# Kernel tuning notes

Hardware: AMD Instinct MI355X
Metric: run time of the kernel (lower is better)

The kernel has to match this reference:

```python
import jax, jax.numpy as jnp
import numpy as np

EPS = 1e-5

def layer_norm(x, gamma, beta):
    mu = jnp.mean(x, axis=-1, keepdims=True)
    var = jnp.mean((x - mu) ** 2, axis=-1, keepdims=True)
    return (x - mu) * jax.lax.rsqrt(var + EPS) * gamma + beta

def setup_inputs() -> dict:
    key = jax.random.key(0)
    ks = jax.random.split(key, 12)
    N, E, D, B = 100000, 1200000, 64, 1
    x_h = jax.random.normal(ks[0], (N, D), dtype=jnp.float32)
    edge_index = jax.random.randint(ks[1], (2, E), 0, N, dtype=jnp.int64)
    edge_attr_h = jax.random.normal(ks[2], (E, D), dtype=jnp.float32)
    u = jax.random.normal(ks[3], (B, 1), dtype=jnp.float32)
    batch = jnp.zeros((N,), dtype=jnp.int64)
    s = 0.05
    W1 = jax.random.normal(ks[4], (2 * D, D), dtype=jnp.float32) * s
    b1 = jnp.zeros((D,), dtype=jnp.float32)
    g1 = jnp.ones((D,), dtype=jnp.float32); be1 = jnp.zeros((D,), dtype=jnp.float32)
    W2 = jax.random.normal(ks[5], (2 * D + 1, D), dtype=jnp.float32) * s
    b2 = jnp.zeros((D,), dtype=jnp.float32)
    g2 = jnp.ones((D,), dtype=jnp.float32); be2 = jnp.zeros((D,), dtype=jnp.float32)
    W3 = jax.random.normal(ks[6], (D, D), dtype=jnp.float32) * s
    b3 = jnp.zeros((D,), dtype=jnp.float32)
    g3 = jnp.ones((D,), dtype=jnp.float32); be3 = jnp.zeros((D,), dtype=jnp.float32)
    return {"x_h": x_h, "edge_index": edge_index, "edge_attr_h": edge_attr_h, "u": u, "batch": batch,
            "W1": W1, "b1": b1, "g1": g1, "be1": be1,
            "W2": W2, "b2": b2, "g2": g2, "be2": be2,
            "W3": W3, "b3": b3, "g3": g3, "be3": be3}

def reference(x_h, edge_index, edge_attr_h, u, batch,
              W1, b1, g1, be1, W2, b2, g2, be2, W3, b3, g3, be3):
    N = x_h.shape[0]
    row, col = edge_index[0], edge_index[1]
    # gather source node features, concat with edge features -> mlp1
    m = jnp.concatenate([x_h[row], edge_attr_h], axis=1)            # [E, 2D]
    m = layer_norm(jax.nn.relu(m @ W1 + b1), g1, be1)               # [E, D]
    # scatter_mean over destination nodes
    summed = jax.ops.segment_sum(m, col, num_segments=N)            # [N, D]
    cnt = jax.ops.segment_sum(jnp.ones((m.shape[0],), m.dtype), col, num_segments=N)
    agg = summed / jnp.maximum(cnt, 1.0)[:, None]                   # [N, D]
    h = jnp.concatenate([x_h, agg, u[batch]], axis=1)               # [N, 2D+1]
    h = layer_norm(jax.nn.relu(h @ W2 + b2), g2, be2)
    h = layer_norm(h @ W3 + b3, g3, be3)
    return h + x_h
```

## Files before the change

### kernel.cpp

```cpp
#include <hip/hip_runtime.h>

#define EPS 1e-5f

typedef __attribute__((ext_vector_type(8))) short short8v;
typedef __attribute__((ext_vector_type(4))) float f32x4;

__device__ __forceinline__ unsigned short f2bf(float f) {
    unsigned u = __builtin_bit_cast(unsigned, f);
    u += 0x7fffu + ((u >> 16) & 1u);
    return (unsigned short)(u >> 16);
}
__device__ __forceinline__ float bf2f(unsigned short h) {
    return __builtin_bit_cast(float, (unsigned)h << 16);
}

__global__ __launch_bounds__(256) void prep_kernel(const float* __restrict__ x,
                                                   unsigned short* __restrict__ xbf,
                                                   float* __restrict__ zbase,
                                                   long zn4, long n8) {
    long i = (long)blockIdx.x * blockDim.x + threadIdx.x;
    long stride = (long)gridDim.x * blockDim.x;
    float4* z4 = (float4*)zbase;
    for (long k = i; k < zn4; k += stride) z4[k] = make_float4(0.f, 0.f, 0.f, 0.f);
    const float4* x4 = (const float4*)x;
    for (long k = i; k < n8; k += stride) {
        float4 a = x4[2 * k], b = x4[2 * k + 1];
        short8v v;
        v[0] = (short)f2bf(a.x); v[1] = (short)f2bf(a.y);
        v[2] = (short)f2bf(a.z); v[3] = (short)f2bf(a.w);
        v[4] = (short)f2bf(b.x); v[5] = (short)f2bf(b.y);
        v[6] = (short)f2bf(b.z); v[7] = (short)f2bf(b.w);
        ((short8v*)xbf)[k] = v;
    }
}

__global__ __launch_bounds__(256) void hist_kernel(const int* __restrict__ col,
                                                   int* __restrict__ cnt, long E) {
    for (long e = (long)blockIdx.x * 256 + threadIdx.x; e < E; e += (long)gridDim.x * 256)
        atomicAdd(&cnt[col[e]], 1);
}

__global__ __launch_bounds__(256) void scan1_kernel(const int* __restrict__ cnt,
                                                    int* __restrict__ offs,
                                                    int* __restrict__ partials, int N) {
    __shared__ int sdata[256];
    int t = threadIdx.x;
    int i0 = blockIdx.x * 1024 + t * 4;
    int c[4]; int tot = 0;
    #pragma unroll
    for (int j = 0; j < 4; ++j) { c[j] = (i0 + j < N) ? cnt[i0 + j] : 0; tot += c[j]; }
    sdata[t] = tot; __syncthreads();
    for (int d = 1; d < 256; d <<= 1) {
        int v = (t >= d) ? sdata[t - d] : 0;
        __syncthreads();
        sdata[t] += v;
        __syncthreads();
    }
    int run = sdata[t] - tot;
    #pragma unroll
    for (int j = 0; j < 4; ++j) { if (i0 + j < N) offs[i0 + j] = run; run += c[j]; }
    if (t == 255) partials[blockIdx.x] = sdata[255];
}

__global__ __launch_bounds__(256) void scan2_kernel(int* __restrict__ partials, int nb) {
    __shared__ int sdata[256];
    int t = threadIdx.x;
    int v = (t < nb) ? partials[t] : 0;
    sdata[t] = v; __syncthreads();
    for (int d = 1; d < 256; d <<= 1) {
        int w = (t >= d) ? sdata[t - d] : 0;
        __syncthreads();
        sdata[t] += w;
        __syncthreads();
    }
    if (t < nb) partials[t] = sdata[t] - v;
}

__global__ __launch_bounds__(256) void scan3_kernel(int* __restrict__ offs,
                                                    int* __restrict__ head,
                                                    const int* __restrict__ partials, int N) {
    int base = partials[blockIdx.x];
    int i0 = blockIdx.x * 1024 + threadIdx.x * 4;
    #pragma unroll
    for (int j = 0; j < 4; ++j) {
        int i = i0 + j;
        if (i < N) { int v = offs[i] + base; offs[i] = v; head[i] = v; }
    }
}

__global__ __launch_bounds__(256) void permscat_kernel(const int* __restrict__ row,
                                                       const int* __restrict__ col,
                                                       int* __restrict__ head,
                                                       int2* __restrict__ einfo,
                                                       int* __restrict__ dsts, long E) {
    for (long e = (long)blockIdx.x * 256 + threadIdx.x; e < E; e += (long)gridDim.x * 256) {
        int cdst = col[e];
        int pos = atomicAdd(&head[cdst], 1);
        einfo[pos] = make_int2((int)e, row[e]);
        dsts[pos] = cdst;
    }
}

__global__ __launch_bounds__(256) void edge_kernel(
    const unsigned short* __restrict__ xbf, const float* __restrict__ eattr,
    const int2* __restrict__ einfo, const int* __restrict__ dsts,
    const float* __restrict__ W1, const float* __restrict__ b1,
    const float* __restrict__ g1, const float* __restrict__ be1,
    unsigned short* __restrict__ summed,
    int E, int N)
{
    __shared__ unsigned short T[4][64][72];
    __shared__ int dseg[4][64];

    const int lane = threadIdx.x & 63;
    const int wid  = threadIdx.x >> 6;
    const int c = lane & 15;
    const int q = lane >> 4;

    short8v w1f[4][4];
    #pragma unroll
    for (int ks = 0; ks < 4; ++ks) {
        #pragma unroll
        for (int nt = 0; nt < 4; ++nt) {
            int k0 = ks * 32 + q * 8;
            int n  = nt * 16 + c;
            short8v f;
            #pragma unroll
            for (int j = 0; j < 8; ++j) f[j] = (short)f2bf(W1[(k0 + j) * 64 + n]);
            w1f[ks][nt] = f;
        }
    }
    float b1v[4], g1v[4], bev[4];
    #pragma unroll
    for (int nt = 0; nt < 4; ++nt) {
        b1v[nt] = b1[nt * 16 + c];
        g1v[nt] = g1[nt * 16 + c];
        bev[nt] = be1[nt * 16 + c];
    }

    for (long e0 = (long)blockIdx.x * 256 + wid * 64; e0 < E; e0 += (long)gridDim.x * 256) {
        long el = e0 + lane;
        bool valid = el < E;
        int2 ps = valid ? einfo[el] : make_int2(0, 0);
        int pe = ps.x;
        int sv = ps.y;
        int dv = valid ? dsts[el] : -1;

        int prev = __shfl_up(dv, 1);
        int seg  = (lane > 0 && dv != prev) ? 1 : 0;
        int rank = seg;
        #pragma unroll
        for (int d = 1; d < 64; d <<= 1) {
            int v = __shfl_up(rank, d);
            if (lane >= d) rank += v;
        }
        int nseg = __shfl(rank, 63) + 1;
        if (lane == 0 || seg) dseg[wid][rank] = dv;

        #pragma unroll
        for (int mt = 0; mt < 4; ++mt) {
            int src  = __shfl(sv, mt * 16 + c);
            int pidx = __shfl(pe, mt * 16 + c);
            const unsigned short* xp = xbf + (long)src * 64;
            const float* ep = eattr + (long)pidx * 64;

            f32x4 acc[4];
            #pragma unroll
            for (int nt = 0; nt < 4; ++nt) acc[nt] = (f32x4){0.f, 0.f, 0.f, 0.f};

            #pragma unroll
            for (int ks = 0; ks < 2; ++ks) {
                short8v a = *(const short8v*)(xp + ks * 32 + q * 8);
                #pragma unroll
                for (int nt = 0; nt < 4; ++nt)
                    acc[nt] = __builtin_amdgcn_mfma_f32_16x16x32_bf16(
                        a, w1f[ks][nt], acc[nt], 0, 0, 0);
            }
            #pragma unroll
            for (int ks = 2; ks < 4; ++ks) {
                int k0 = (ks - 2) * 32 + q * 8;
                float4 lo = *(const float4*)(ep + k0);
                float4 hi = *(const float4*)(ep + k0 + 4);
                short8v a;
                a[0] = (short)f2bf(lo.x); a[1] = (short)f2bf(lo.y);
                a[2] = (short)f2bf(lo.z); a[3] = (short)f2bf(lo.w);
                a[4] = (short)f2bf(hi.x); a[5] = (short)f2bf(hi.y);
                a[6] = (short)f2bf(hi.z); a[7] = (short)f2bf(hi.w);
                #pragma unroll
                for (int nt = 0; nt < 4; ++nt)
                    acc[nt] = __builtin_amdgcn_mfma_f32_16x16x32_bf16(
                        a, w1f[ks][nt], acc[nt], 0, 0, 0);
            }

            float s1[4] = {0, 0, 0, 0}, s2[4] = {0, 0, 0, 0};
            #pragma unroll
            for (int nt = 0; nt < 4; ++nt)
                #pragma unroll
                for (int r = 0; r < 4; ++r) {
                    float f = fmaxf(acc[nt][r] + b1v[nt], 0.f);
                    acc[nt][r] = f;
                    s1[r] += f; s2[r] += f * f;
                }
            #pragma unroll
            for (int m = 1; m <= 8; m <<= 1)
                #pragma unroll
                for (int r = 0; r < 4; ++r) {
                    s1[r] += __shfl_xor(s1[r], m);
                    s2[r] += __shfl_xor(s2[r], m);
                }
            #pragma unroll
            for (int r = 0; r < 4; ++r) {
                float mu = s1[r] * (1.f / 64.f);
                float var = s2[r] * (1.f / 64.f) - mu * mu;
                float rs = rsqrtf(var + EPS);
                #pragma unroll
                for (int nt = 0; nt < 4; ++nt) {
                    float h = (acc[nt][r] - mu) * rs * g1v[nt] + bev[nt];
                    T[wid][nt * 16 + c][mt * 16 + q * 4 + r] = f2bf(h);
                }
            }
        }

        short8v bfr[2][4];
        #pragma unroll
        for (int ks = 0; ks < 2; ++ks)
            #pragma unroll
            for (int nt = 0; nt < 4; ++nt)
                bfr[ks][nt] = *(const short8v*)&T[wid][nt * 16 + c][ks * 32 + q * 8];

        const short ONE = (short)0x3F80;
        #pragma unroll
        for (int mt = 0; mt < 4; ++mt) {
            if (mt * 16 < nseg) {
                f32x4 acc2[4];
                #pragma unroll
                for (int nt = 0; nt < 4; ++nt) acc2[nt] = (f32x4){0.f, 0.f, 0.f, 0.f};

                #pragma unroll
                for (int ks = 0; ks < 2; ++ks) {
                    short8v af;
                    #pragma unroll
                    for (int j = 0; j < 8; ++j) {
                        int rk = __shfl(rank, ks * 32 + q * 8 + j);
                        af[j] = (rk == mt * 16 + c) ? ONE : (short)0;
                    }
                    #pragma unroll
                    for (int nt = 0; nt < 4; ++nt)
                        acc2[nt] = __builtin_amdgcn_mfma_f32_16x16x32_bf16(
                            af, bfr[ks][nt], acc2[nt], 0, 0, 0);
                }

                #pragma unroll
                for (int r = 0; r < 4; ++r) {
                    int s = mt * 16 + q * 4 + r;
                    #pragma unroll
                    for (int nt = 0; nt < 4; ++nt) {
                        float val = acc2[nt][r];
                        float nb = __shfl_xor(val, 1);
                        if (s < nseg && !(c & 1)) {
                            int dst = dseg[wid][s];
                            if (dst >= 0) {
                                unsigned pk = (unsigned)f2bf(val) | ((unsigned)f2bf(nb) << 16);
                                unsigned long long a64 = (unsigned long long)
                                    (summed + (long)dst * 64 + nt * 16 + c);
                                asm volatile("global_atomic_pk_add_bf16 %0, %1, off"
                                             :: "v"(a64), "v"(pk));
                            }
                        }
                    }
                }
            }
        }
    }
}

__global__ __launch_bounds__(256) void node_kernel(
    const float* __restrict__ x_h, const float* __restrict__ u,
    const float* __restrict__ W2, const float* __restrict__ b2,
    const float* __restrict__ g2, const float* __restrict__ be2,
    const float* __restrict__ W3, const float* __restrict__ b3,
    const float* __restrict__ g3, const float* __restrict__ be3,
    const unsigned short* __restrict__ summed, const int* __restrict__ cnt,
    float* __restrict__ out, int N)
{
    __shared__ unsigned short sh[4][64][72];

    const int lane = threadIdx.x & 63;
    const int wid  = threadIdx.x >> 6;
    const int c = lane & 15;
    const int q = lane >> 4;
    const float u0 = u[0];

    short8v w2f[4][4], w3f[2][4];
    #pragma unroll
    for (int ks = 0; ks < 4; ++ks)
        #pragma unroll
        for (int nt = 0; nt < 4; ++nt) {
            int k0 = ks * 32 + q * 8;
            int n  = nt * 16 + c;
            short8v f;
            #pragma unroll
            for (int j = 0; j < 8; ++j) f[j] = (short)f2bf(W2[(k0 + j) * 64 + n]);
            w2f[ks][nt] = f;
        }
    #pragma unroll
    for (int ks = 0; ks < 2; ++ks)
        #pragma unroll
        for (int nt = 0; nt < 4; ++nt) {
            int k0 = ks * 32 + q * 8;
            int n  = nt * 16 + c;
            short8v f;
            #pragma unroll
            for (int j = 0; j < 8; ++j) f[j] = (short)f2bf(W3[(k0 + j) * 64 + n]);
            w3f[ks][nt] = f;
        }

    float b2p[4], g2v[4], be2v[4], b3v[4], g3v[4], be3v[4];
    #pragma unroll
    for (int nt = 0; nt < 4; ++nt) {
        int n = nt * 16 + c;
        b2p[nt] = b2[n] + u0 * W2[128 * 64 + n];
        g2v[nt] = g2[n]; be2v[nt] = be2[n];
        b3v[nt] = b3[n]; g3v[nt] = g3[n]; be3v[nt] = be3[n];
    }

    const long n0 = ((long)blockIdx.x * 4 + wid) * 64;
    if (n0 >= N) return;

    #pragma unroll
    for (int mt = 0; mt < 4; ++mt) {
        long nr = n0 + mt * 16 + c;
        long nc = (nr < N) ? nr : (N - 1);
        const float* xp = x_h + nc * 64;
        const unsigned short* sp = summed + nc * 64;
        float inv = 1.f / fmaxf((float)cnt[nc], 1.f);

        f32x4 acc[4];
        #pragma unroll
        for (int nt = 0; nt < 4; ++nt) acc[nt] = (f32x4){0.f, 0.f, 0.f, 0.f};

        #pragma unroll
        for (int ks = 0; ks < 4; ++ks) {
            int k0 = ks * 32 + q * 8;
            short8v a;
            if (ks < 2) {
                float4 lo = *(const float4*)(xp + k0);
                float4 hi = *(const float4*)(xp + k0 + 4);
                a[0] = (short)f2bf(lo.x); a[1] = (short)f2bf(lo.y);
                a[2] = (short)f2bf(lo.z); a[3] = (short)f2bf(lo.w);
                a[4] = (short)f2bf(hi.x); a[5] = (short)f2bf(hi.y);
                a[6] = (short)f2bf(hi.z); a[7] = (short)f2bf(hi.w);
            } else {
                short8v raw = *(const short8v*)(sp + (k0 - 64));
                #pragma unroll
                for (int j = 0; j < 8; ++j)
                    a[j] = (short)f2bf(bf2f((unsigned short)raw[j]) * inv);
            }
            #pragma unroll
            for (int nt = 0; nt < 4; ++nt)
                acc[nt] = __builtin_amdgcn_mfma_f32_16x16x32_bf16(a, w2f[ks][nt], acc[nt], 0, 0, 0);
        }

        float s1[4] = {0, 0, 0, 0}, s2[4] = {0, 0, 0, 0};
        #pragma unroll
        for (int nt = 0; nt < 4; ++nt)
            #pragma unroll
            for (int r = 0; r < 4; ++r) {
                float f = fmaxf(acc[nt][r] + b2p[nt], 0.f);
                acc[nt][r] = f;
                s1[r] += f; s2[r] += f * f;
            }
        #pragma unroll
        for (int m = 1; m <= 8; m <<= 1)
            #pragma unroll
            for (int r = 0; r < 4; ++r) {
                s1[r] += __shfl_xor(s1[r], m);
                s2[r] += __shfl_xor(s2[r], m);
            }
        #pragma unroll
        for (int r = 0; r < 4; ++r) {
            float mu = s1[r] * (1.f / 64.f);
            float var = s2[r] * (1.f / 64.f) - mu * mu;
            float rs = rsqrtf(var + EPS);
            #pragma unroll
            for (int nt = 0; nt < 4; ++nt) {
                float h2 = (acc[nt][r] - mu) * rs * g2v[nt] + be2v[nt];
                sh[wid][mt * 16 + q * 4 + r][nt * 16 + c] = f2bf(h2);
            }
        }
    }

    #pragma unroll
    for (int mt = 0; mt < 4; ++mt) {
        f32x4 acc[4];
        #pragma unroll
        for (int nt = 0; nt < 4; ++nt) acc[nt] = (f32x4){0.f, 0.f, 0.f, 0.f};

        #pragma unroll
        for (int ks = 0; ks < 2; ++ks) {
            short8v a = *(const short8v*)&sh[wid][mt * 16 + c][ks * 32 + q * 8];
            #pragma unroll
            for (int nt = 0; nt < 4; ++nt)
                acc[nt] = __builtin_amdgcn_mfma_f32_16x16x32_bf16(a, w3f[ks][nt], acc[nt], 0, 0, 0);
        }

        float s1[4] = {0, 0, 0, 0}, s2[4] = {0, 0, 0, 0};
        #pragma unroll
        for (int nt = 0; nt < 4; ++nt)
            #pragma unroll
            for (int r = 0; r < 4; ++r) {
                float f = acc[nt][r] + b3v[nt];
                acc[nt][r] = f;
                s1[r] += f; s2[r] += f * f;
            }
        #pragma unroll
        for (int m = 1; m <= 8; m <<= 1)
            #pragma unroll
            for (int r = 0; r < 4; ++r) {
                s1[r] += __shfl_xor(s1[r], m);
                s2[r] += __shfl_xor(s2[r], m);
            }
        #pragma unroll
        for (int r = 0; r < 4; ++r) {
            float mu = s1[r] * (1.f / 64.f);
            float var = s2[r] * (1.f / 64.f) - mu * mu;
            float rs = rsqrtf(var + EPS);
            long node = n0 + mt * 16 + q * 4 + r;
            if (node < N) {
                #pragma unroll
                for (int nt = 0; nt < 4; ++nt) {
                    long off = node * 64 + nt * 16 + c;
                    float h3 = (acc[nt][r] - mu) * rs * g3v[nt] + be3v[nt];
                    out[off] = h3 + x_h[off];
                }
            }
        }
    }
}

extern "C" void kernel_launch(void* const* d_in, const int* in_sizes, int n_in,
                              void* d_out, int out_size, void* d_ws, size_t ws_size,
                              hipStream_t stream)
{
    const float* x_h   = (const float*)d_in[0];
    const int*   eidx  = (const int*)  d_in[1];
    const float* eattr = (const float*)d_in[2];
    const float* u     = (const float*)d_in[3];
    const float* W1  = (const float*)d_in[5];
    const float* b1  = (const float*)d_in[6];
    const float* g1  = (const float*)d_in[7];
    const float* be1 = (const float*)d_in[8];
    const float* W2  = (const float*)d_in[9];
    const float* b2  = (const float*)d_in[10];
    const float* g2  = (const float*)d_in[11];
    const float* be2 = (const float*)d_in[12];
    const float* W3  = (const float*)d_in[13];
    const float* b3  = (const float*)d_in[14];
    const float* g3  = (const float*)d_in[15];
    const float* be3 = (const float*)d_in[16];

    const int N = in_sizes[0] / 64;
    const int E = in_sizes[1] / 2;
    const int* row = eidx;
    const int* col = eidx + E;

    char* w = (char*)d_ws;
    unsigned short* xbf    = (unsigned short*)w;   w += (size_t)N * 128;
    unsigned short* summed = (unsigned short*)w;   w += (size_t)N * 128;
    int* cnt      = (int*)w;                       w += (size_t)N * 4;
    int* offs     = (int*)w;                       w += (size_t)N * 4;
    int* head     = (int*)w;                       w += (size_t)N * 4;
    int* dsts     = (int*)w;                       w += (size_t)E * 4;
    int2* einfo   = (int2*)w;                      w += (size_t)E * 8;
    int* partials = (int*)w;

    prep_kernel<<<1024, 256, 0, stream>>>(x_h, xbf, (float*)summed, ((long)N * 33) / 4, (long)N * 8);

    hist_kernel<<<2048, 256, 0, stream>>>(col, cnt, E);
    int sblocks = (N + 1023) / 1024;
    scan1_kernel<<<sblocks, 256, 0, stream>>>(cnt, offs, partials, N);
    scan2_kernel<<<1, 256, 0, stream>>>(partials, sblocks);
    scan3_kernel<<<sblocks, 256, 0, stream>>>(offs, head, partials, N);
    permscat_kernel<<<2048, 256, 0, stream>>>(row, col, head, einfo, dsts, E);

    int tiles = (E + 63) / 64;
    int eblocks = (tiles + 7) / 8;
    edge_kernel<<<eblocks, 256, 0, stream>>>(xbf, eattr, einfo, dsts,
                                             W1, b1, g1, be1, summed, E, N);

    int nblocks = (N + 255) / 256;
    node_kernel<<<nblocks, 256, 0, stream>>>(x_h, u, W2, b2, g2, be2, W3, b3, g3, be3,
                                             summed, cnt, (float*)d_out, N);
}
```

Baseline: 358.8 us.

## Split edge MLP from aggregation; compute MLP in original edge order, aggregate sorted

After: 330.8 us. 7.8% less time.

```diff
diff --git a/kernel.cpp b/kernel.cpp
--- a/kernel.cpp
+++ b/kernel.cpp
@@ -88,11 +88,23 @@
     }
 }
 
-__global__ __launch_bounds__(256) void permscat_kernel(const int* __restrict__ row,
-                                                       const int* __restrict__ col,
-                                                       int* __restrict__ head,
-                                                       int2* __restrict__ einfo,
-                                                       int* __restrict__ dsts, long E) {
+__global__ __launch_bounds__(256) void permscat2_kernel(const int* __restrict__ col,
+                                                        int* __restrict__ head,
+                                                        int* __restrict__ perm,
+                                                        int* __restrict__ dsts, long E) {
+    for (long e = (long)blockIdx.x * 256 + threadIdx.x; e < E; e += (long)gridDim.x * 256) {
+        int cdst = col[e];
+        int pos = atomicAdd(&head[cdst], 1);
+        perm[pos] = (int)e;
+        dsts[pos] = cdst;
+    }
+}
+
+__global__ __launch_bounds__(256) void permscat_r9_kernel(const int* __restrict__ row,
+                                                          const int* __restrict__ col,
+                                                          int* __restrict__ head,
+                                                          int2* __restrict__ einfo,
+                                                          int* __restrict__ dsts, long E) {
     for (long e = (long)blockIdx.x * 256 + threadIdx.x; e < E; e += (long)gridDim.x * 256) {
         int cdst = col[e];
         int pos = atomicAdd(&head[cdst], 1);
@@ -101,7 +113,164 @@
     }
 }
 
-__global__ __launch_bounds__(256) void edge_kernel(
+__global__ __launch_bounds__(256) void mlp_kernel(
+    const unsigned short* __restrict__ xbf, const int* __restrict__ eidx,
+    const float* __restrict__ eattr,
+    const float* __restrict__ W1, const float* __restrict__ b1,
+    const float* __restrict__ g1, const float* __restrict__ be1,
+    unsigned short* __restrict__ m, int* __restrict__ cnt, int E)
+{
+    const int lane = threadIdx.x & 63;
+    const int wid  = threadIdx.x >> 6;
+    const int c = lane & 15;
+    const int q = lane >> 4;
+
+    short8v w1f[4][4];
+    #pragma unroll
+    for (int ks = 0; ks < 4; ++ks)
+        #pragma unroll
+        for (int nt = 0; nt < 4; ++nt) {
+            int k0 = ks * 32 + q * 8;
+            int n  = nt * 16 + c;
+            short8v f;
+            #pragma unroll
+            for (int j = 0; j < 8; ++j) f[j] = (short)f2bf(W1[(k0 + j) * 64 + n]);
+            w1f[ks][nt] = f;
+        }
+    float b1v[4], g1v[4], bev[4];
+    #pragma unroll
+    for (int nt = 0; nt < 4; ++nt) {
+        b1v[nt] = b1[nt * 16 + c];
+        g1v[nt] = g1[nt * 16 + c];
+        bev[nt] = be1[nt * 16 + c];
+    }
+
+    for (long e0 = (long)blockIdx.x * 256 + wid * 64; e0 < E; e0 += (long)gridDim.x * 256) {
+        int sv_l;
+        {
+            long el = e0 + lane;
+            if (el < E) atomicAdd(&cnt[eidx[E + el]], 1);
+            sv_l = (el < E) ? eidx[el] : 0;
+        }
+
+        #pragma unroll
+        for (int mt = 0; mt < 4; ++mt) {
+            long er = e0 + mt * 16 + c;
+            long ec = (er < E) ? er : (E - 1);
+            int src = __shfl(sv_l, mt * 16 + c);
+            const unsigned short* xp = xbf + (long)src * 64;
+            const float* ep = eattr + ec * 64;
+
+            f32x4 acc[4];
+            #pragma unroll
+            for (int nt = 0; nt < 4; ++nt) acc[nt] = (f32x4){0.f, 0.f, 0.f, 0.f};
+
+            #pragma unroll
+            for (int ks = 0; ks < 2; ++ks) {
+                short8v a = *(const short8v*)(xp + ks * 32 + q * 8);
+                #pragma unroll
+                for (int nt = 0; nt < 4; ++nt)
+                    acc[nt] = __builtin_amdgcn_mfma_f32_16x16x32_bf16(
+                        a, w1f[ks][nt], acc[nt], 0, 0, 0);
+            }
+            #pragma unroll
+            for (int ks = 2; ks < 4; ++ks) {
+                int k0 = (ks - 2) * 32 + q * 8;
+                float4 lo = *(const float4*)(ep + k0);
+                float4 hi = *(const float4*)(ep + k0 + 4);
+                short8v a;
+                a[0] = (short)f2bf(lo.x); a[1] = (short)f2bf(lo.y);
+                a[2] = (short)f2bf(lo.z); a[3] = (short)f2bf(lo.w);
+                a[4] = (short)f2bf(hi.x); a[5] = (short)f2bf(hi.y);
+                a[6] = (short)f2bf(hi.z); a[7] = (short)f2bf(hi.w);
+                #pragma unroll
+                for (int nt = 0; nt < 4; ++nt)
+                    acc[nt] = __builtin_amdgcn_mfma_f32_16x16x32_bf16(
+                        a, w1f[ks][nt], acc[nt], 0, 0, 0);
+            }
+
+            float s1[4] = {0, 0, 0, 0}, s2[4] = {0, 0, 0, 0};
+            #pragma unroll
+            for (int nt = 0; nt < 4; ++nt)
+                #pragma unroll
+                for (int r = 0; r < 4; ++r) {
+                    float f = fmaxf(acc[nt][r] + b1v[nt], 0.f);
+                    acc[nt][r] = f;
+                    s1[r] += f; s2[r] += f * f;
+                }
+            #pragma unroll
+            for (int mm = 1; mm <= 8; mm <<= 1)
+                #pragma unroll
+                for (int r = 0; r < 4; ++r) {
+                    s1[r] += __shfl_xor(s1[r], mm);
+                    s2[r] += __shfl_xor(s2[r], mm);
+                }
+            #pragma unroll
+            for (int r = 0; r < 4; ++r) {
+                float mu = s1[r] * (1.f / 64.f);
+                float var = s2[r] * (1.f / 64.f) - mu * mu;
+                float rs = rsqrtf(var + EPS);
+                long ee = e0 + mt * 16 + q * 4 + r;
+                #pragma unroll
+                for (int nt = 0; nt < 4; ++nt) {
+                    float h = (acc[nt][r] - mu) * rs * g1v[nt] + bev[nt];
+                    float nb = __shfl_xor(h, 1);
+                    if (ee < E && !(c & 1)) {
+                        unsigned pk = (unsigned)f2bf(h) | ((unsigned)f2bf(nb) << 16);
+                        *(unsigned*)(m + ee * 64 + nt * 16 + c) = pk;
+                    }
+                }
+            }
+        }
+    }
+}
+
+__global__ __launch_bounds__(256, 8) void agg_kernel(
+    const unsigned short* __restrict__ m, const int* __restrict__ perm,
+    const int* __restrict__ dsts, unsigned short* __restrict__ summed, int E)
+{
+    const int lane = threadIdx.x & 63;
+    const int wid  = threadIdx.x >> 6;
+
+    for (long s0 = ((long)blockIdx.x * 4 + wid) * 64; s0 < E; s0 += (long)gridDim.x * 256) {
+        long sl = s0 + lane;
+        int pe_l = (sl < E) ? perm[sl] : 0;
+        int dv_l = (sl < E) ? dsts[sl] : -1;
+
+        float acc = 0.f;
+        #pragma unroll
+        for (int base = 0; base < 64; base += 8) {
+            int pe8[8], dv8[8]; float v[8];
+            #pragma unroll
+            for (int j = 0; j < 8; ++j) {
+                pe8[j] = __shfl(pe_l, base + j);
+                dv8[j] = __shfl(dv_l, base + j);
+            }
+            int dvn = (base < 56) ? __shfl(dv_l, base + 8) : (int)0x80000000;
+            #pragma unroll
+            for (int j = 0; j < 8; ++j)
+                v[j] = bf2f(m[(long)pe8[j] * 64 + lane]);
+            #pragma unroll
+            for (int j = 0; j < 8; ++j) {
+                if (dv8[j] >= 0) acc += v[j];
+                int nxt = (j < 7) ? dv8[j + 1] : dvn;
+                if (nxt != dv8[j]) {
+                    float nb = __shfl_xor(acc, 1);
+                    if (dv8[j] >= 0 && !(lane & 1)) {
+                        unsigned pk = (unsigned)f2bf(acc) | ((unsigned)f2bf(nb) << 16);
+                        unsigned long long a64 = (unsigned long long)
+                            (summed + (long)dv8[j] * 64 + lane);
+                        asm volatile("global_atomic_pk_add_bf16 %0, %1, off"
+                                     :: "v"(a64), "v"(pk));
+                    }
+                    acc = 0.f;
+                }
+            }
+        }
+    }
+}
+
+__global__ __launch_bounds__(256) void edge_kernel_r9(
     const unsigned short* __restrict__ xbf, const float* __restrict__ eattr,
     const int2* __restrict__ einfo, const int* __restrict__ dsts,
     const float* __restrict__ W1, const float* __restrict__ b1,
@@ -119,7 +288,7 @@
 
     short8v w1f[4][4];
     #pragma unroll
-    for (int ks = 0; ks < 4; ++ks) {
+    for (int ks = 0; ks < 4; ++ks)
         #pragma unroll
         for (int nt = 0; nt < 4; ++nt) {
             int k0 = ks * 32 + q * 8;
@@ -129,7 +298,6 @@
             for (int j = 0; j < 8; ++j) f[j] = (short)f2bf(W1[(k0 + j) * 64 + n]);
             w1f[ks][nt] = f;
         }
-    }
     float b1v[4], g1v[4], bev[4];
     #pragma unroll
     for (int nt = 0; nt < 4; ++nt) {
@@ -142,8 +310,7 @@
         long el = e0 + lane;
         bool valid = el < E;
         int2 ps = valid ? einfo[el] : make_int2(0, 0);
-        int pe = ps.x;
-        int sv = ps.y;
+        int pe = ps.x, sv = ps.y;
         int dv = valid ? dsts[el] : -1;
 
         int prev = __shfl_up(dv, 1);
@@ -202,11 +369,11 @@
                     s1[r] += f; s2[r] += f * f;
                 }
             #pragma unroll
-            for (int m = 1; m <= 8; m <<= 1)
+            for (int mmm = 1; mmm <= 8; mmm <<= 1)
                 #pragma unroll
                 for (int r = 0; r < 4; ++r) {
-                    s1[r] += __shfl_xor(s1[r], m);
-                    s2[r] += __shfl_xor(s2[r], m);
+                    s1[r] += __shfl_xor(s1[r], mmm);
+                    s2[r] += __shfl_xor(s2[r], mmm);
                 }
             #pragma unroll
             for (int r = 0; r < 4; ++r) {
@@ -235,7 +402,6 @@
                 f32x4 acc2[4];
                 #pragma unroll
                 for (int nt = 0; nt < 4; ++nt) acc2[nt] = (f32x4){0.f, 0.f, 0.f, 0.f};
-
                 #pragma unroll
                 for (int ks = 0; ks < 2; ++ks) {
                     short8v af;
@@ -249,7 +415,6 @@
                         acc2[nt] = __builtin_amdgcn_mfma_f32_16x16x32_bf16(
                             af, bfr[ks][nt], acc2[nt], 0, 0, 0);
                 }
-
                 #pragma unroll
                 for (int r = 0; r < 4; ++r) {
                     int s = mt * 16 + q * 4 + r;
@@ -371,11 +536,11 @@
                 s1[r] += f; s2[r] += f * f;
             }
         #pragma unroll
-        for (int m = 1; m <= 8; m <<= 1)
+        for (int mm = 1; mm <= 8; mm <<= 1)
             #pragma unroll
             for (int r = 0; r < 4; ++r) {
-                s1[r] += __shfl_xor(s1[r], m);
-                s2[r] += __shfl_xor(s2[r], m);
+                s1[r] += __shfl_xor(s1[r], mm);
+                s2[r] += __shfl_xor(s2[r], mm);
             }
         #pragma unroll
         for (int r = 0; r < 4; ++r) {
@@ -414,11 +579,11 @@
                 s1[r] += f; s2[r] += f * f;
             }
         #pragma unroll
-        for (int m = 1; m <= 8; m <<= 1)
+        for (int mm = 1; mm <= 8; mm <<= 1)
             #pragma unroll
             for (int r = 0; r < 4; ++r) {
-                s1[r] += __shfl_xor(s1[r], m);
-                s2[r] += __shfl_xor(s2[r], m);
+                s1[r] += __shfl_xor(s1[r], mm);
+                s2[r] += __shfl_xor(s2[r], mm);
             }
         #pragma unroll
         for (int r = 0; r < 4; ++r) {
@@ -464,31 +629,60 @@
     const int* row = eidx;
     const int* col = eidx + E;
 
-    char* w = (char*)d_ws;
-    unsigned short* xbf    = (unsigned short*)w;   w += (size_t)N * 128;
-    unsigned short* summed = (unsigned short*)w;   w += (size_t)N * 128;
-    int* cnt      = (int*)w;                       w += (size_t)N * 4;
-    int* offs     = (int*)w;                       w += (size_t)N * 4;
-    int* head     = (int*)w;                       w += (size_t)N * 4;
-    int* dsts     = (int*)w;                       w += (size_t)E * 4;
-    int2* einfo   = (int2*)w;                      w += (size_t)E * 8;
-    int* partials = (int*)w;
-
-    prep_kernel<<<1024, 256, 0, stream>>>(x_h, xbf, (float*)summed, ((long)N * 33) / 4, (long)N * 8);
-
-    hist_kernel<<<2048, 256, 0, stream>>>(col, cnt, E);
-    int sblocks = (N + 1023) / 1024;
-    scan1_kernel<<<sblocks, 256, 0, stream>>>(cnt, offs, partials, N);
-    scan2_kernel<<<1, 256, 0, stream>>>(partials, sblocks);
-    scan3_kernel<<<sblocks, 256, 0, stream>>>(offs, head, partials, N);
-    permscat_kernel<<<2048, 256, 0, stream>>>(row, col, head, einfo, dsts, E);
-
-    int tiles = (E + 63) / 64;
-    int eblocks = (tiles + 7) / 8;
-    edge_kernel<<<eblocks, 256, 0, stream>>>(xbf, eattr, einfo, dsts,
-                                             W1, b1, g1, be1, summed, E, N);
-
-    int nblocks = (N + 255) / 256;
-    node_kernel<<<nblocks, 256, 0, stream>>>(x_h, u, W2, b2, g2, be2, W3, b3, g3, be3,
-                                             summed, cnt, (float*)d_out, N);
-}
+    size_t need = (size_t)N * 268 + (size_t)E * 8 + (size_t)E * 128 + 4096;
+
+    if (ws_size >= need) {
+        char* w = (char*)d_ws;
+        unsigned short* xbf    = (unsigned short*)w;   w += (size_t)N * 128;
+        unsigned short* summed = (unsigned short*)w;   w += (size_t)N * 128;
+        int* cnt      = (int*)w;                       w += (size_t)N * 4;
+        int* offs     = (int*)w;                       w += (size_t)N * 4;
+        int* head     = (int*)w;                       w += (size_t)N * 4;
+        int* perm     = (int*)w;                       w += (size_t)E * 4;
+        int* dsts     = (int*)w;                       w += (size_t)E * 4;
+        unsigned short* m = (unsigned short*)w;        w += (size_t)E * 128;
+        int* partials = (int*)w;
+
+        prep_kernel<<<1024, 256, 0, stream>>>(x_h, xbf, (float*)summed,
+                                              ((long)N * 33) / 4, (long)N * 8);
+        mlp_kernel<<<2048, 256, 0, stream>>>(xbf, eidx, eattr, W1, b1, g1, be1,
+                                             m, cnt, E);
+        int sblocks = (N + 1023) / 1024;
+        scan1_kernel<<<sblocks, 256, 0, stream>>>(cnt, offs, partials, N);
+        scan2_kernel<<<1, 256, 0, stream>>>(partials, sblocks);
+        scan3_kernel<<<sblocks, 256, 0, stream>>>(offs, head, partials, N);
+        permscat2_kernel<<<2048, 256, 0, stream>>>(col, head, perm, dsts, E);
+        agg_kernel<<<2048, 256, 0, stream>>>(m, perm, dsts, summed, E);
+
+        int nblocks = (N + 255) / 256;
+        node_kernel<<<nblocks, 256, 0, stream>>>(x_h, u, W2, b2, g2, be2, W3, b3, g3, be3,
+                                                 summed, cnt, (float*)d_out, N);
+    } else {
+        char* w = (char*)d_ws;
+        unsigned short* xbf    = (unsigned short*)w;   w += (size_t)N * 128;
+        unsigned short* summed = (unsigned short*)w;   w += (size_t)N * 128;
+        int* cnt      = (int*)w;                       w += (size_t)N * 4;
+        int* offs     = (int*)w;                       w += (size_t)N * 4;
+        int* head     = (int*)w;                       w += (size_t)N * 4;
+        int* dsts     = (int*)w;                       w += (size_t)E * 4;
+        int2* einfo   = (int2*)w;                      w += (size_t)E * 8;
+        int* partials = (int*)w;
+
+        prep_kernel<<<1024, 256, 0, stream>>>(x_h, xbf, (float*)summed,
+                                              ((long)N * 33) / 4, (long)N * 8);
+        hist_kernel<<<2048, 256, 0, stream>>>(col, cnt, E);
+        int sblocks = (N + 1023) / 1024;
+        scan1_kernel<<<sblocks, 256, 0, stream>>>(cnt, offs, partials, N);
+        scan2_kernel<<<1, 256, 0, stream>>>(partials, sblocks);
+        scan3_kernel<<<sblocks, 256, 0, stream>>>(offs, head, partials, N);
+        permscat_r9_kernel<<<2048, 256, 0, stream>>>(row, col, head, einfo, dsts, E);
+
+        int tiles = (E + 63) / 64;
+        int eblocks = (tiles + 7) / 8;
+        edge_kernel_r9<<<eblocks, 256, 0, stream>>>(xbf, eattr, einfo, dsts,
+                                                    W1, b1, g1, be1, summed, E, N);
+        int nblocks = (N + 255) / 256;
+        node_kernel<<<nblocks, 256, 0, stream>>>(x_h, u, W2, b2, g2, be2, W3, b3, g3, be3,
+                                                 summed, cnt, (float*)d_out, N);
+    }
+}
```
